# Optimization experiments

Hardware: AMD Instinct MI355X
Metric: run time of the kernel (lower is better)

## Reference

```python
import jax, jax.numpy as jnp
import numpy as np
import math

N = 4096          # ld_num == number of tokens (forced by downsampling Linear over token axis)
D = 640           # input_dim
H = 4             # head_num
E = 16            # per-head output_dim (hardcoded in module)
N_OUT = N // 2    # ld_num // dsp_scale


def setup_inputs() -> dict:
    key = jax.random.key(0)
    ks = jax.random.split(key, 9)
    s = 0.02
    return {
        "x":  jax.random.normal(ks[0], (N, D), dtype=jnp.float32),
        "Wq": jax.random.normal(ks[1], (H, E, D), dtype=jnp.float32) * s,
        "bq": jax.random.normal(ks[2], (H, E), dtype=jnp.float32) * s,
        "Wk": jax.random.normal(ks[3], (H, E, D), dtype=jnp.float32) * s,
        "bk": jax.random.normal(ks[4], (H, E), dtype=jnp.float32) * s,
        "Wv": jax.random.normal(ks[5], (H, E, D), dtype=jnp.float32) * s,
        "bv": jax.random.normal(ks[6], (H, E), dtype=jnp.float32) * s,
        "Wd": jax.random.normal(ks[7], (N_OUT, N), dtype=jnp.float32) * s,
        "bd": jax.random.normal(ks[8], (N_OUT,), dtype=jnp.float32) * s,
    }


def reference(x, Wq, bq, Wk, bk, Wv, bv, Wd, bd):
    # Batched per-head QKV projections: [H, N, E]
    q = jnp.einsum('nd,hed->hne', x, Wq) + bq[:, None, :]
    k = jnp.einsum('nd,hed->hne', x, Wk) + bk[:, None, :]
    v = jnp.einsum('nd,hed->hne', x, Wv) + bv[:, None, :]
    scale = 1.0 / math.sqrt(E)
    attn = jax.nn.softmax(jnp.einsum('hne,hme->hnm', q, k) * scale, axis=-1)  # [H,N,N]
    v = v + jnp.einsum('hnm,hme->hne', attn, v)  # residual + attention readout
    # Concat heads along feature dim: [N, H*E]
    V = jnp.transpose(v, (1, 0, 2)).reshape(N, H * E)
    # downsampling Linear over the token axis, then transpose back: [N//2, H*E]
    out = Wd @ V + bd[:, None]
    return out
```

## Files before the change

### kernel.cpp

```cpp
#include <hip/hip_runtime.h>

typedef __bf16 bf16x8 __attribute__((ext_vector_type(8)));
typedef __bf16 bf16x4 __attribute__((ext_vector_type(4)));
typedef short s16x4 __attribute__((ext_vector_type(4)));
typedef float f32x4 __attribute__((ext_vector_type(4)));

#define MFMA32(a, b, c) __builtin_amdgcn_mfma_f32_16x16x32_bf16((a), (b), (c), 0, 0, 0)
#define MFMA16(a, b, c) __builtin_amdgcn_mfma_f32_16x16x16bf16_1k((a), (b), (c), 0, 0, 0)

#define QSCALE 0.36067376022224085f

static __device__ inline bf16x8 cvt8(float4 a, float4 b) {
    bf16x8 r;
    r[0] = (__bf16)a.x; r[1] = (__bf16)a.y; r[2] = (__bf16)a.z; r[3] = (__bf16)a.w;
    r[4] = (__bf16)b.x; r[5] = (__bf16)b.y; r[6] = (__bf16)b.z; r[7] = (__bf16)b.w;
    return r;
}

__global__ __launch_bounds__(256) void qkv_kernel(
    const float* __restrict__ x,
    const float* __restrict__ Wq, const float* __restrict__ bq,
    const float* __restrict__ Wk, const float* __restrict__ bk,
    const float* __restrict__ Wv, const float* __restrict__ bv,
    const float* __restrict__ bd,
    __bf16* __restrict__ q_bf, __bf16* __restrict__ k_bf,
    __bf16* __restrict__ vT_t, float* __restrict__ out)
{
    __shared__ float red[4 * 4 * 64 * 4];

    const int rg = blockIdx.x & 255;
    const int which = blockIdx.x >> 8;
    const int w  = threadIdx.x >> 6;
    const int lane = threadIdx.x & 63;
    const int c = lane & 15;
    const int g = lane >> 4;
    const int row0 = rg << 4;

    if (which == 0) {
        const int tid0 = (rg << 8) + threadIdx.x;
        const float b = bd[tid0 >> 5];
        *(float2*)(out + (tid0 << 1)) = make_float2(b, b);
    }

    const float* Wsel = (which == 0) ? Wq : (which == 1) ? Wk : Wv;
    const float* bsel = (which == 0) ? bq : (which == 1) ? bk : bv;

    const float* xrow = x + (row0 + c) * 640 + w * 160;
    const float* wr0 = Wsel + (0 * 16 + c) * 640 + w * 160;
    const float* wr1 = Wsel + (1 * 16 + c) * 640 + w * 160;
    const float* wr2 = Wsel + (2 * 16 + c) * 640 + w * 160;
    const float* wr3 = Wsel + (3 * 16 + c) * 640 + w * 160;

    f32x4 acc0 = {0.f,0.f,0.f,0.f}, acc1 = acc0, acc2 = acc0, acc3 = acc0;
    #pragma unroll 5
    for (int k0 = 0; k0 < 160; k0 += 32) {
        const int kk = k0 + (g << 3);
        bf16x8 af = cvt8(*(const float4*)(xrow + kk), *(const float4*)(xrow + kk + 4));
        bf16x8 b0 = cvt8(*(const float4*)(wr0 + kk), *(const float4*)(wr0 + kk + 4));
        bf16x8 b1 = cvt8(*(const float4*)(wr1 + kk), *(const float4*)(wr1 + kk + 4));
        bf16x8 b2 = cvt8(*(const float4*)(wr2 + kk), *(const float4*)(wr2 + kk + 4));
        bf16x8 b3 = cvt8(*(const float4*)(wr3 + kk), *(const float4*)(wr3 + kk + 4));
        acc0 = MFMA32(af, b0, acc0);
        acc1 = MFMA32(af, b1, acc1);
        acc2 = MFMA32(af, b2, acc2);
        acc3 = MFMA32(af, b3, acc3);
    }

    *(f32x4*)&red[((((w << 2) + 0) << 6) + lane) << 2] = acc0;
    *(f32x4*)&red[((((w << 2) + 1) << 6) + lane) << 2] = acc1;
    *(f32x4*)&red[((((w << 2) + 2) << 6) + lane) << 2] = acc2;
    *(f32x4*)&red[((((w << 2) + 3) << 6) + lane) << 2] = acc3;
    __syncthreads();

    const int h = threadIdx.x >> 6;
    f32x4 sum = {0.f,0.f,0.f,0.f};
    #pragma unroll
    for (int ww = 0; ww < 4; ++ww)
        sum += *(const f32x4*)&red[((((ww << 2) + h) << 6) + lane) << 2];

    const float bias = bsel[(h << 4) + c];
    if (which == 2) {
        bf16x4 vv;
        #pragma unroll
        for (int i = 0; i < 4; ++i) vv[i] = (__bf16)(sum[i] + bias);
        *(bf16x4*)(vT_t + ((((h << 8) + rg) << 8) + (c << 4) + (g << 2))) = vv;
    } else {
        #pragma unroll
        for (int i = 0; i < 4; ++i) {
            const int n = row0 + (g << 2) + i;
            const float val = sum[i] + bias;
            if (which == 0) q_bf[(((h << 12) + n) << 4) + c] = (__bf16)(val * QSCALE);
            else            k_bf[(((h << 12) + n) << 4) + c] = (__bf16)val;
        }
    }
}

__global__ __launch_bounds__(512) void attn_kernel(
    const __bf16* __restrict__ q_bf, const __bf16* __restrict__ k_bf,
    const __bf16* __restrict__ vT_t, __bf16* __restrict__ voutT)
{
    __shared__ float accl[8 * 2 * 256];
    __shared__ float lred[8 * 2 * 16];
    __shared__ float ltot[2 * 16];

    const int bx = blockIdx.x;
    const int qp = bx & 127;
    const int h  = bx >> 7;
    const int tid = threadIdx.x;
    const int w = tid >> 6;
    const int lane = tid & 63;
    const int c = lane & 15;
    const int g = lane >> 4;
    const int qbase = qp << 5;

    const s16x4 qf0 = *(const s16x4*)(q_bf + (((h << 12) + qbase + c) << 4) + (g << 2));
    const s16x4 qf1 = *(const s16x4*)(q_bf + (((h << 12) + qbase + 16 + c) << 4) + (g << 2));

    const __bf16* kb = k_bf + (((h << 12) + (w << 9)) << 4) + (c << 4) + (g << 2);
    const __bf16* vb = vT_t + (((h << 8) + (w << 5)) << 8) + (c << 4) + (g << 2);

    bf16x4 one4;
    #pragma unroll
    for (int j = 0; j < 4; ++j) one4[j] = (__bf16)1.0f;
    const s16x4 onesf = __builtin_bit_cast(s16x4, one4);

    const f32x4 z = {0.f, 0.f, 0.f, 0.f};
    f32x4 acc0 = z, acc1 = z, la0 = z, la1 = z;

    s16x4 kr0 = *(const s16x4*)(kb);
    s16x4 kr1 = *(const s16x4*)(kb + 256);
    s16x4 kr2 = *(const s16x4*)(kb + 512);
    s16x4 kr3 = *(const s16x4*)(kb + 768);
    s16x4 vr0 = *(const s16x4*)(vb);
    s16x4 vr1 = *(const s16x4*)(vb + 256);
    s16x4 vr2 = *(const s16x4*)(vb + 512);
    s16x4 vr3 = *(const s16x4*)(vb + 768);

#define ATTN_BODY(KC, VC)                                                     \
    {                                                                         \
        f32x4 s0 = MFMA16((KC), qf0, z);                                      \
        f32x4 s1 = MFMA16((KC), qf1, z);                                      \
        float p00 = __builtin_amdgcn_exp2f(s0[0]);                            \
        float p01 = __builtin_amdgcn_exp2f(s0[1]);                            \
        float p02 = __builtin_amdgcn_exp2f(s0[2]);                            \
        float p03 = __builtin_amdgcn_exp2f(s0[3]);                            \
        float p10 = __builtin_amdgcn_exp2f(s1[0]);                            \
        float p11 = __builtin_amdgcn_exp2f(s1[1]);                            \
        float p12 = __builtin_amdgcn_exp2f(s1[2]);                            \
        float p13 = __builtin_amdgcn_exp2f(s1[3]);                            \
        bf16x4 pb0, pb1;                                                      \
        pb0[0] = (__bf16)p00; pb0[1] = (__bf16)p01;                           \
        pb0[2] = (__bf16)p02; pb0[3] = (__bf16)p03;                           \
        pb1[0] = (__bf16)p10; pb1[1] = (__bf16)p11;                           \
        pb1[2] = (__bf16)p12; pb1[3] = (__bf16)p13;                           \
        const s16x4 pf0 = __builtin_bit_cast(s16x4, pb0);                     \
        const s16x4 pf1 = __builtin_bit_cast(s16x4, pb1);                     \
        la0 = MFMA16(onesf, pf0, la0);                                        \
        la1 = MFMA16(onesf, pf1, la1);                                        \
        acc0 = MFMA16((VC), pf0, acc0);                                       \
        acc1 = MFMA16((VC), pf1, acc1);                                       \
    }

    for (int tt = 0; tt < 32; tt += 4) {
        s16x4 kc, vc;
        kc = kr0; vc = vr0;
        if (tt + 4 < 32) { kr0 = *(const s16x4*)(kb + ((tt + 4) << 8)); vr0 = *(const s16x4*)(vb + ((tt + 4) << 8)); }
        ATTN_BODY(kc, vc)
        kc = kr1; vc = vr1;
        if (tt + 5 < 32) { kr1 = *(const s16x4*)(kb + ((tt + 5) << 8)); vr1 = *(const s16x4*)(vb + ((tt + 5) << 8)); }
        ATTN_BODY(kc, vc)
        kc = kr2; vc = vr2;
        if (tt + 6 < 32) { kr2 = *(const s16x4*)(kb + ((tt + 6) << 8)); vr2 = *(const s16x4*)(vb + ((tt + 6) << 8)); }
        ATTN_BODY(kc, vc)
        kc = kr3; vc = vr3;
        if (tt + 7 < 32) { kr3 = *(const s16x4*)(kb + ((tt + 7) << 8)); vr3 = *(const s16x4*)(vb + ((tt + 7) << 8)); }
        ATTN_BODY(kc, vc)
    }
#undef ATTN_BODY

    *(f32x4*)&accl[(((w << 1) + 0) << 8) + (lane << 2)] = acc0;
    *(f32x4*)&accl[(((w << 1) + 1) << 8) + (lane << 2)] = acc1;
    if (g == 0) {
        lred[(((w << 1) + 0) << 4) + c] = la0[0];
        lred[(((w << 1) + 1) << 4) + c] = la1[0];
    }
    __syncthreads();

    if (tid < 32) {
        const int tile = tid >> 4, cc = tid & 15;
        float s = 0.f;
        #pragma unroll
        for (int w2 = 0; w2 < 8; ++w2) s += lred[(((w2 << 1) + tile) << 4) + cc];
        ltot[(tile << 4) + cc] = 1.0f / s;
    }
    __syncthreads();

    {
        const int tile = tid >> 8;
        const int elem = tid & 255;
        const int lane2 = elem >> 2, i = elem & 3;
        const int c2 = lane2 & 15, g2 = lane2 >> 4;
        const int e = (g2 << 2) + i;
        float s = 0.f;
        #pragma unroll
        for (int w2 = 0; w2 < 8; ++w2) s += accl[(((w2 << 1) + tile) << 8) + elem];
        const int qt = (qp << 1) + tile;
        const float res = (float)vT_t[((((h << 8) + qt) << 8)) + (e << 4) + c2];
        const float val = s * ltot[(tile << 4) + c2] + res;
        voutT[(qp << 11) + (((h << 4) + e) << 5) + (tile << 4) + c2] = (__bf16)val;
    }
}

__global__ __launch_bounds__(256) void dsgemm_kernel(
    const float* __restrict__ Wd, const __bf16* __restrict__ voutT,
    float* __restrict__ out)
{
    const int rb = blockIdx.x & 31;
    const int ks = blockIdx.x >> 5;
    const int w  = threadIdx.x >> 6;
    const int lane = threadIdx.x & 63;
    const int c = lane & 15;
    const int g = lane >> 4;
    const int rowbase = rb * 64 + w * 16;
    const float* wdrow = Wd + (rowbase + c) * 4096;

    f32x4 acc0 = {0.f,0.f,0.f,0.f}, acc1 = acc0, acc2 = acc0, acc3 = acc0;
    #pragma unroll
    for (int it = 0; it < 8; ++it) {
        const int k0 = ks * 256 + it * 32;
        bf16x8 af = cvt8(*(const float4*)(wdrow + k0 + (g << 3)),
                         *(const float4*)(wdrow + k0 + (g << 3) + 4));
        const __bf16* bt = voutT + ((k0 >> 5) << 11) + (g << 3);
        bf16x8 b0 = *(const bf16x8*)(bt + ((c     ) << 5));
        bf16x8 b1 = *(const bf16x8*)(bt + ((c + 16) << 5));
        bf16x8 b2 = *(const bf16x8*)(bt + ((c + 32) << 5));
        bf16x8 b3 = *(const bf16x8*)(bt + ((c + 48) << 5));
        acc0 = MFMA32(af, b0, acc0);
        acc1 = MFMA32(af, b1, acc1);
        acc2 = MFMA32(af, b2, acc2);
        acc3 = MFMA32(af, b3, acc3);
    }

    float* ob = out + rowbase * 64;
    #pragma unroll
    for (int i = 0; i < 4; ++i) {
        const int r = (g << 2) + i;
        atomicAdd(ob + r * 64 +      c, acc0[i]);
        atomicAdd(ob + r * 64 + 16 + c, acc1[i]);
        atomicAdd(ob + r * 64 + 32 + c, acc2[i]);
        atomicAdd(ob + r * 64 + 48 + c, acc3[i]);
    }
}

extern "C" void kernel_launch(void* const* d_in, const int* in_sizes, int n_in,
                              void* d_out, int out_size, void* d_ws, size_t ws_size,
                              hipStream_t stream)
{
    const float* x  = (const float*)d_in[0];
    const float* Wq = (const float*)d_in[1];
    const float* bq = (const float*)d_in[2];
    const float* Wk = (const float*)d_in[3];
    const float* bk = (const float*)d_in[4];
    const float* Wv = (const float*)d_in[5];
    const float* bv = (const float*)d_in[6];
    const float* Wd = (const float*)d_in[7];
    const float* bd = (const float*)d_in[8];
    float* out = (float*)d_out;

    char* ws = (char*)d_ws;
    __bf16* q_bf   = (__bf16*)(ws);
    __bf16* k_bf   = (__bf16*)(ws + (1u << 19));
    __bf16* vT_t   = (__bf16*)(ws + (2u << 19));
    __bf16* voutT  = (__bf16*)(ws + (3u << 19));

    qkv_kernel<<<dim3(768), dim3(256), 0, stream>>>(x, Wq, bq, Wk, bk, Wv, bv, bd,
                                                    q_bf, k_bf, vT_t, out);
    attn_kernel<<<dim3(512), dim3(512), 0, stream>>>(q_bf, k_bf, vT_t, voutT);
    dsgemm_kernel<<<dim3(512), dim3(256), 0, stream>>>(Wd, voutT, out);
}
```

Baseline: 51.51 us.

## Fuse QKV, attention and downsample GEMM into one persistent kernel with grid barriers

Replaces the three launches with a single 256-block persistent kernel. Software grid barriers on atomic counters separate the phases. The QKV phase stages x rows in LDS and computes all three projections per block. Attention blocks now handle 64 queries each instead of 32, and the downsample GEMM writes per-k-split partials that a final phase reduces with the bias, replacing atomicAdd. The aim is to cut launch gaps and atomic contention, at the cost of barrier spin time, an extra memset, lower block parallelism and reliance on all 256 blocks being co-resident.

```diff
diff --git a/kernel.cpp b/kernel.cpp
--- a/kernel.cpp
+++ b/kernel.cpp
@@ -17,238 +17,289 @@
     return r;
 }
 
-__global__ __launch_bounds__(256) void qkv_kernel(
+static __device__ inline void grid_barrier(unsigned* cnt, int nblk) {
+    __syncthreads();
+    if (threadIdx.x == 0) {
+        __threadfence();
+        unsigned prev = __hip_atomic_fetch_add(cnt, 1u, __ATOMIC_ACQ_REL,
+                                               __HIP_MEMORY_SCOPE_AGENT);
+        if ((int)prev + 1 < nblk) {
+            int guard = 0;
+            while (__hip_atomic_load(cnt, __ATOMIC_ACQUIRE,
+                                     __HIP_MEMORY_SCOPE_AGENT) < (unsigned)nblk) {
+                __builtin_amdgcn_s_sleep(8);
+                if (++guard > (1 << 22)) break;
+            }
+        }
+        __threadfence();
+    }
+    __syncthreads();
+}
+
+__global__ __launch_bounds__(512) void fused_kernel(
     const float* __restrict__ x,
     const float* __restrict__ Wq, const float* __restrict__ bq,
     const float* __restrict__ Wk, const float* __restrict__ bk,
     const float* __restrict__ Wv, const float* __restrict__ bv,
-    const float* __restrict__ bd,
+    const float* __restrict__ Wd, const float* __restrict__ bd,
     __bf16* __restrict__ q_bf, __bf16* __restrict__ k_bf,
-    __bf16* __restrict__ vT_t, float* __restrict__ out)
+    __bf16* __restrict__ vT_t, __bf16* __restrict__ voutT,
+    float* __restrict__ partial, unsigned* __restrict__ bars,
+    float* __restrict__ out)
 {
-    __shared__ float red[4 * 4 * 64 * 4];
-
-    const int rg = blockIdx.x & 255;
-    const int which = blockIdx.x >> 8;
-    const int w  = threadIdx.x >> 6;
-    const int lane = threadIdx.x & 63;
-    const int c = lane & 15;
-    const int g = lane >> 4;
-    const int row0 = rg << 4;
-
-    if (which == 0) {
-        const int tid0 = (rg << 8) + threadIdx.x;
-        const float b = bd[tid0 >> 5];
-        *(float2*)(out + (tid0 << 1)) = make_float2(b, b);
-    }
-
-    const float* Wsel = (which == 0) ? Wq : (which == 1) ? Wk : Wv;
-    const float* bsel = (which == 0) ? bq : (which == 1) ? bk : bv;
-
-    const float* xrow = x + (row0 + c) * 640 + w * 160;
-    const float* wr0 = Wsel + (0 * 16 + c) * 640 + w * 160;
-    const float* wr1 = Wsel + (1 * 16 + c) * 640 + w * 160;
-    const float* wr2 = Wsel + (2 * 16 + c) * 640 + w * 160;
-    const float* wr3 = Wsel + (3 * 16 + c) * 640 + w * 160;
-
-    f32x4 acc0 = {0.f,0.f,0.f,0.f}, acc1 = acc0, acc2 = acc0, acc3 = acc0;
-    #pragma unroll 5
-    for (int k0 = 0; k0 < 160; k0 += 32) {
-        const int kk = k0 + (g << 3);
-        bf16x8 af = cvt8(*(const float4*)(xrow + kk), *(const float4*)(xrow + kk + 4));
-        bf16x8 b0 = cvt8(*(const float4*)(wr0 + kk), *(const float4*)(wr0 + kk + 4));
-        bf16x8 b1 = cvt8(*(const float4*)(wr1 + kk), *(const float4*)(wr1 + kk + 4));
-        bf16x8 b2 = cvt8(*(const float4*)(wr2 + kk), *(const float4*)(wr2 + kk + 4));
-        bf16x8 b3 = cvt8(*(const float4*)(wr3 + kk), *(const float4*)(wr3 + kk + 4));
-        acc0 = MFMA32(af, b0, acc0);
-        acc1 = MFMA32(af, b1, acc1);
-        acc2 = MFMA32(af, b2, acc2);
-        acc3 = MFMA32(af, b3, acc3);
-    }
-
-    *(f32x4*)&red[((((w << 2) + 0) << 6) + lane) << 2] = acc0;
-    *(f32x4*)&red[((((w << 2) + 1) << 6) + lane) << 2] = acc1;
-    *(f32x4*)&red[((((w << 2) + 2) << 6) + lane) << 2] = acc2;
-    *(f32x4*)&red[((((w << 2) + 3) << 6) + lane) << 2] = acc3;
-    __syncthreads();
-
-    const int h = threadIdx.x >> 6;
-    f32x4 sum = {0.f,0.f,0.f,0.f};
-    #pragma unroll
-    for (int ww = 0; ww < 4; ++ww)
-        sum += *(const f32x4*)&red[((((ww << 2) + h) << 6) + lane) << 2];
-
-    const float bias = bsel[(h << 4) + c];
-    if (which == 2) {
-        bf16x4 vv;
-        #pragma unroll
-        for (int i = 0; i < 4; ++i) vv[i] = (__bf16)(sum[i] + bias);
-        *(bf16x4*)(vT_t + ((((h << 8) + rg) << 8) + (c << 4) + (g << 2))) = vv;
-    } else {
-        #pragma unroll
-        for (int i = 0; i < 4; ++i) {
-            const int n = row0 + (g << 2) + i;
-            const float val = sum[i] + bias;
-            if (which == 0) q_bf[(((h << 12) + n) << 4) + c] = (__bf16)(val * QSCALE);
-            else            k_bf[(((h << 12) + n) << 4) + c] = (__bf16)val;
-        }
-    }
-}
-
-__global__ __launch_bounds__(512) void attn_kernel(
-    const __bf16* __restrict__ q_bf, const __bf16* __restrict__ k_bf,
-    const __bf16* __restrict__ vT_t, __bf16* __restrict__ voutT)
-{
-    __shared__ float accl[8 * 2 * 256];
-    __shared__ float lred[8 * 2 * 16];
-    __shared__ float ltot[2 * 16];
-
-    const int bx = blockIdx.x;
-    const int qp = bx & 127;
-    const int h  = bx >> 7;
+    __shared__ __align__(16) char arena[67584];
+
     const int tid = threadIdx.x;
     const int w = tid >> 6;
     const int lane = tid & 63;
     const int c = lane & 15;
     const int g = lane >> 4;
-    const int qbase = qp << 5;
-
-    const s16x4 qf0 = *(const s16x4*)(q_bf + (((h << 12) + qbase + c) << 4) + (g << 2));
-    const s16x4 qf1 = *(const s16x4*)(q_bf + (((h << 12) + qbase + 16 + c) << 4) + (g << 2));
-
-    const __bf16* kb = k_bf + (((h << 12) + (w << 9)) << 4) + (c << 4) + (g << 2);
-    const __bf16* vb = vT_t + (((h << 8) + (w << 5)) << 8) + (c << 4) + (g << 2);
-
-    bf16x4 one4;
-    #pragma unroll
-    for (int j = 0; j < 4; ++j) one4[j] = (__bf16)1.0f;
-    const s16x4 onesf = __builtin_bit_cast(s16x4, one4);
-
-    const f32x4 z = {0.f, 0.f, 0.f, 0.f};
-    f32x4 acc0 = z, acc1 = z, la0 = z, la1 = z;
-
-    s16x4 kr0 = *(const s16x4*)(kb);
-    s16x4 kr1 = *(const s16x4*)(kb + 256);
-    s16x4 kr2 = *(const s16x4*)(kb + 512);
-    s16x4 kr3 = *(const s16x4*)(kb + 768);
-    s16x4 vr0 = *(const s16x4*)(vb);
-    s16x4 vr1 = *(const s16x4*)(vb + 256);
-    s16x4 vr2 = *(const s16x4*)(vb + 512);
-    s16x4 vr3 = *(const s16x4*)(vb + 768);
-
+
+    {
+        const int rg = blockIdx.x;
+        const int row0 = rg << 4;
+        float* xs = (float*)arena;
+        f32x4* red = (f32x4*)(arena + 41216);
+
+        const float4* xg = (const float4*)(x + row0 * 640);
+        #pragma unroll
+        for (int i = 0; i < 5; ++i) {
+            const int j = tid + (i << 9);
+            const int row = j / 160, col = j - row * 160;
+            *(float4*)&xs[row * 644 + (col << 2)] = xg[j];
+        }
+        __syncthreads();
+
+        if (w < 6) {
+            const int which = w >> 1, kh = w & 1;
+            const float* Wsel = which == 0 ? Wq : which == 1 ? Wk : Wv;
+            const float* wr0 = Wsel + (0 * 16 + c) * 640 + kh * 320;
+            const float* wr1 = Wsel + (1 * 16 + c) * 640 + kh * 320;
+            const float* wr2 = Wsel + (2 * 16 + c) * 640 + kh * 320;
+            const float* wr3 = Wsel + (3 * 16 + c) * 640 + kh * 320;
+            const float* xr = xs + c * 644 + kh * 320;
+
+            f32x4 acc0 = {0.f,0.f,0.f,0.f}, acc1 = acc0, acc2 = acc0, acc3 = acc0;
+            #pragma unroll 2
+            for (int it = 0; it < 10; ++it) {
+                const int kk = (it << 5) + (g << 3);
+                bf16x8 af = cvt8(*(const float4*)(xr + kk), *(const float4*)(xr + kk + 4));
+                bf16x8 b0 = cvt8(*(const float4*)(wr0 + kk), *(const float4*)(wr0 + kk + 4));
+                bf16x8 b1 = cvt8(*(const float4*)(wr1 + kk), *(const float4*)(wr1 + kk + 4));
+                bf16x8 b2 = cvt8(*(const float4*)(wr2 + kk), *(const float4*)(wr2 + kk + 4));
+                bf16x8 b3 = cvt8(*(const float4*)(wr3 + kk), *(const float4*)(wr3 + kk + 4));
+                acc0 = MFMA32(af, b0, acc0);
+                acc1 = MFMA32(af, b1, acc1);
+                acc2 = MFMA32(af, b2, acc2);
+                acc3 = MFMA32(af, b3, acc3);
+            }
+            red[((w << 2) + 0) * 64 + lane] = acc0;
+            red[((w << 2) + 1) * 64 + lane] = acc1;
+            red[((w << 2) + 2) * 64 + lane] = acc2;
+            red[((w << 2) + 3) * 64 + lane] = acc3;
+        }
+        __syncthreads();
+
+        #pragma unroll
+        for (int pass = 0; pass < 2; ++pass) {
+            const int s = tid + (pass << 9);
+            if (s < 768) {
+                const int which = s >> 8;
+                const int h = (s >> 6) & 3;
+                const int ln = s & 63;
+                const int cc = ln & 15, gg = ln >> 4;
+                f32x4 sum = red[(((which << 1) << 2) + h) * 64 + ln]
+                          + red[((((which << 1) + 1) << 2) + h) * 64 + ln];
+                const float* bsel = which == 0 ? bq : which == 1 ? bk : bv;
+                const float bias = bsel[(h << 4) + cc];
+                if (which == 2) {
+                    bf16x4 vv;
+                    #pragma unroll
+                    for (int i = 0; i < 4; ++i) vv[i] = (__bf16)(sum[i] + bias);
+                    *(bf16x4*)(vT_t + ((((h << 8) + rg) << 8) + (cc << 4) + (gg << 2))) = vv;
+                } else {
+                    #pragma unroll
+                    for (int i = 0; i < 4; ++i) {
+                        const int n = row0 + (gg << 2) + i;
+                        const float val = sum[i] + bias;
+                        if (which == 0) q_bf[(((h << 12) + n) << 4) + cc] = (__bf16)(val * QSCALE);
+                        else            k_bf[(((h << 12) + n) << 4) + cc] = (__bf16)val;
+                    }
+                }
+            }
+        }
+    }
+    grid_barrier(bars + 0, 256);
+
+    {
+        const int h = blockIdx.x >> 6;
+        const int qblk = blockIdx.x & 63;
+        float* accl = (float*)arena;
+        float* lred = (float*)(arena + 32768);
+        float* ltot = (float*)(arena + 34816);
+
+        const int qt0 = qblk << 2;
+        const __bf16* qb = q_bf + (h << 16) + (((qblk << 6) + c) << 4) + (g << 2);
+        const s16x4 qf0 = *(const s16x4*)(qb);
+        const s16x4 qf1 = *(const s16x4*)(qb + 256);
+        const s16x4 qf2 = *(const s16x4*)(qb + 512);
+        const s16x4 qf3 = *(const s16x4*)(qb + 768);
+
+        const __bf16* kb = k_bf + (h << 16) + (w << 13) + (c << 4) + (g << 2);
+        const __bf16* vb = vT_t + (h << 16) + (w << 13) + (c << 4) + (g << 2);
+
+        bf16x4 one4;
+        #pragma unroll
+        for (int j = 0; j < 4; ++j) one4[j] = (__bf16)1.0f;
+        const s16x4 onesf = __builtin_bit_cast(s16x4, one4);
+
+        const f32x4 z = {0.f, 0.f, 0.f, 0.f};
+        f32x4 acc0 = z, acc1 = z, acc2 = z, acc3 = z;
+        f32x4 la0 = z, la1 = z, la2 = z, la3 = z;
+
+        s16x4 kr0 = *(const s16x4*)(kb);
+        s16x4 kr1 = *(const s16x4*)(kb + 256);
+        s16x4 kr2 = *(const s16x4*)(kb + 512);
+        s16x4 kr3 = *(const s16x4*)(kb + 768);
+        s16x4 vr0 = *(const s16x4*)(vb);
+        s16x4 vr1 = *(const s16x4*)(vb + 256);
+        s16x4 vr2 = *(const s16x4*)(vb + 512);
+        s16x4 vr3 = *(const s16x4*)(vb + 768);
+
+#define TILE_OP(QF, ACC, LA, KC, VC)                                          \
+        {                                                                     \
+            f32x4 s_ = MFMA16((KC), (QF), z);                                 \
+            float p0 = __builtin_amdgcn_exp2f(s_[0]);                         \
+            float p1 = __builtin_amdgcn_exp2f(s_[1]);                         \
+            float p2 = __builtin_amdgcn_exp2f(s_[2]);                         \
+            float p3 = __builtin_amdgcn_exp2f(s_[3]);                         \
+            bf16x4 pb;                                                        \
+            pb[0] = (__bf16)p0; pb[1] = (__bf16)p1;                           \
+            pb[2] = (__bf16)p2; pb[3] = (__bf16)p3;                           \
+            const s16x4 pf = __builtin_bit_cast(s16x4, pb);                   \
+            (LA)  = MFMA16(onesf, pf, (LA));                                  \
+            (ACC) = MFMA16((VC), pf, (ACC));                                  \
+        }
 #define ATTN_BODY(KC, VC)                                                     \
-    {                                                                         \
-        f32x4 s0 = MFMA16((KC), qf0, z);                                      \
-        f32x4 s1 = MFMA16((KC), qf1, z);                                      \
-        float p00 = __builtin_amdgcn_exp2f(s0[0]);                            \
-        float p01 = __builtin_amdgcn_exp2f(s0[1]);                            \
-        float p02 = __builtin_amdgcn_exp2f(s0[2]);                            \
-        float p03 = __builtin_amdgcn_exp2f(s0[3]);                            \
-        float p10 = __builtin_amdgcn_exp2f(s1[0]);                            \
-        float p11 = __builtin_amdgcn_exp2f(s1[1]);                            \
-        float p12 = __builtin_amdgcn_exp2f(s1[2]);                            \
-        float p13 = __builtin_amdgcn_exp2f(s1[3]);                            \
-        bf16x4 pb0, pb1;                                                      \
-        pb0[0] = (__bf16)p00; pb0[1] = (__bf16)p01;                           \
-        pb0[2] = (__bf16)p02; pb0[3] = (__bf16)p03;                           \
-        pb1[0] = (__bf16)p10; pb1[1] = (__bf16)p11;                           \
-        pb1[2] = (__bf16)p12; pb1[3] = (__bf16)p13;                           \
-        const s16x4 pf0 = __builtin_bit_cast(s16x4, pb0);                     \
-        const s16x4 pf1 = __builtin_bit_cast(s16x4, pb1);                     \
-        la0 = MFMA16(onesf, pf0, la0);                                        \
-        la1 = MFMA16(onesf, pf1, la1);                                        \
-        acc0 = MFMA16((VC), pf0, acc0);                                       \
-        acc1 = MFMA16((VC), pf1, acc1);                                       \
-    }
-
-    for (int tt = 0; tt < 32; tt += 4) {
-        s16x4 kc, vc;
-        kc = kr0; vc = vr0;
-        if (tt + 4 < 32) { kr0 = *(const s16x4*)(kb + ((tt + 4) << 8)); vr0 = *(const s16x4*)(vb + ((tt + 4) << 8)); }
-        ATTN_BODY(kc, vc)
-        kc = kr1; vc = vr1;
-        if (tt + 5 < 32) { kr1 = *(const s16x4*)(kb + ((tt + 5) << 8)); vr1 = *(const s16x4*)(vb + ((tt + 5) << 8)); }
-        ATTN_BODY(kc, vc)
-        kc = kr2; vc = vr2;
-        if (tt + 6 < 32) { kr2 = *(const s16x4*)(kb + ((tt + 6) << 8)); vr2 = *(const s16x4*)(vb + ((tt + 6) << 8)); }
-        ATTN_BODY(kc, vc)
-        kc = kr3; vc = vr3;
-        if (tt + 7 < 32) { kr3 = *(const s16x4*)(kb + ((tt + 7) << 8)); vr3 = *(const s16x4*)(vb + ((tt + 7) << 8)); }
-        ATTN_BODY(kc, vc)
-    }
+        TILE_OP(qf0, acc0, la0, KC, VC)                                       \
+        TILE_OP(qf1, acc1, la1, KC, VC)                                       \
+        TILE_OP(qf2, acc2, la2, KC, VC)                                       \
+        TILE_OP(qf3, acc3, la3, KC, VC)
+
+        for (int tt = 0; tt < 32; tt += 4) {
+            s16x4 kc, vc;
+            kc = kr0; vc = vr0;
+            if (tt + 4 < 32) { kr0 = *(const s16x4*)(kb + ((tt + 4) << 8)); vr0 = *(const s16x4*)(vb + ((tt + 4) << 8)); }
+            ATTN_BODY(kc, vc)
+            kc = kr1; vc = vr1;
+            if (tt + 5 < 32) { kr1 = *(const s16x4*)(kb + ((tt + 5) << 8)); vr1 = *(const s16x4*)(vb + ((tt + 5) << 8)); }
+            ATTN_BODY(kc, vc)
+            kc = kr2; vc = vr2;
+            if (tt + 6 < 32) { kr2 = *(const s16x4*)(kb + ((tt + 6) << 8)); vr2 = *(const s16x4*)(vb + ((tt + 6) << 8)); }
+            ATTN_BODY(kc, vc)
+            kc = kr3; vc = vr3;
+            if (tt + 7 < 32) { kr3 = *(const s16x4*)(kb + ((tt + 7) << 8)); vr3 = *(const s16x4*)(vb + ((tt + 7) << 8)); }
+            ATTN_BODY(kc, vc)
+        }
 #undef ATTN_BODY
-
-    *(f32x4*)&accl[(((w << 1) + 0) << 8) + (lane << 2)] = acc0;
-    *(f32x4*)&accl[(((w << 1) + 1) << 8) + (lane << 2)] = acc1;
-    if (g == 0) {
-        lred[(((w << 1) + 0) << 4) + c] = la0[0];
-        lred[(((w << 1) + 1) << 4) + c] = la1[0];
-    }
-    __syncthreads();
-
-    if (tid < 32) {
-        const int tile = tid >> 4, cc = tid & 15;
-        float s = 0.f;
-        #pragma unroll
-        for (int w2 = 0; w2 < 8; ++w2) s += lred[(((w2 << 1) + tile) << 4) + cc];
-        ltot[(tile << 4) + cc] = 1.0f / s;
-    }
-    __syncthreads();
+#undef TILE_OP
+
+        *(f32x4*)&accl[(((w << 2) + 0) << 8) + (lane << 2)] = acc0;
+        *(f32x4*)&accl[(((w << 2) + 1) << 8) + (lane << 2)] = acc1;
+        *(f32x4*)&accl[(((w << 2) + 2) << 8) + (lane << 2)] = acc2;
+        *(f32x4*)&accl[(((w << 2) + 3) << 8) + (lane << 2)] = acc3;
+        if (g == 0) {
+            lred[(((w << 2) + 0) << 4) + c] = la0[0];
+            lred[(((w << 2) + 1) << 4) + c] = la1[0];
+            lred[(((w << 2) + 2) << 4) + c] = la2[0];
+            lred[(((w << 2) + 3) << 4) + c] = la3[0];
+        }
+        __syncthreads();
+
+        if (tid < 64) {
+            const int tile = tid >> 4, cc2 = tid & 15;
+            float s = 0.f;
+            #pragma unroll
+            for (int w2 = 0; w2 < 8; ++w2) s += lred[(((w2 << 2) + tile) << 4) + cc2];
+            ltot[tid] = 1.0f / s;
+        }
+        __syncthreads();
+
+        #pragma unroll
+        for (int pass = 0; pass < 2; ++pass) {
+            const int s = tid + (pass << 9);
+            const int tile = s >> 8, elem = s & 255;
+            const int lane2 = elem >> 2, ii = elem & 3;
+            const int c2 = lane2 & 15, g2 = lane2 >> 4;
+            const int e = (g2 << 2) + ii;
+            float ssum = 0.f;
+            #pragma unroll
+            for (int w2 = 0; w2 < 8; ++w2) ssum += accl[(((w2 << 2) + tile) << 8) + elem];
+            const int qt = qt0 + tile;
+            const float res = (float)vT_t[(((h << 8) + qt) << 8) + (e << 4) + c2];
+            const float val = ssum * ltot[(tile << 4) + c2] + res;
+            voutT[((qt >> 1) << 11) + (((h << 4) + e) << 5) + ((qt & 1) << 4) + c2] = (__bf16)val;
+        }
+    }
+    grid_barrier(bars + 16, 256);
 
     {
-        const int tile = tid >> 8;
-        const int elem = tid & 255;
-        const int lane2 = elem >> 2, i = elem & 3;
-        const int c2 = lane2 & 15, g2 = lane2 >> 4;
-        const int e = (g2 << 2) + i;
-        float s = 0.f;
-        #pragma unroll
-        for (int w2 = 0; w2 < 8; ++w2) s += accl[(((w2 << 1) + tile) << 8) + elem];
-        const int qt = (qp << 1) + tile;
-        const float res = (float)vT_t[((((h << 8) + qt) << 8)) + (e << 4) + c2];
-        const float val = s * ltot[(tile << 4) + c2] + res;
-        voutT[(qp << 11) + (((h << 4) + e) << 5) + (tile << 4) + c2] = (__bf16)val;
-    }
-}
-
-__global__ __launch_bounds__(256) void dsgemm_kernel(
-    const float* __restrict__ Wd, const __bf16* __restrict__ voutT,
-    float* __restrict__ out)
-{
-    const int rb = blockIdx.x & 31;
-    const int ks = blockIdx.x >> 5;
-    const int w  = threadIdx.x >> 6;
-    const int lane = threadIdx.x & 63;
-    const int c = lane & 15;
-    const int g = lane >> 4;
-    const int rowbase = rb * 64 + w * 16;
-    const float* wdrow = Wd + (rowbase + c) * 4096;
-
-    f32x4 acc0 = {0.f,0.f,0.f,0.f}, acc1 = acc0, acc2 = acc0, acc3 = acc0;
-    #pragma unroll
-    for (int it = 0; it < 8; ++it) {
-        const int k0 = ks * 256 + it * 32;
-        bf16x8 af = cvt8(*(const float4*)(wdrow + k0 + (g << 3)),
-                         *(const float4*)(wdrow + k0 + (g << 3) + 4));
-        const __bf16* bt = voutT + ((k0 >> 5) << 11) + (g << 3);
-        bf16x8 b0 = *(const bf16x8*)(bt + ((c     ) << 5));
-        bf16x8 b1 = *(const bf16x8*)(bt + ((c + 16) << 5));
-        bf16x8 b2 = *(const bf16x8*)(bt + ((c + 32) << 5));
-        bf16x8 b3 = *(const bf16x8*)(bt + ((c + 48) << 5));
-        acc0 = MFMA32(af, b0, acc0);
-        acc1 = MFMA32(af, b1, acc1);
-        acc2 = MFMA32(af, b2, acc2);
-        acc3 = MFMA32(af, b3, acc3);
-    }
-
-    float* ob = out + rowbase * 64;
-    #pragma unroll
-    for (int i = 0; i < 4; ++i) {
-        const int r = (g << 2) + i;
-        atomicAdd(ob + r * 64 +      c, acc0[i]);
-        atomicAdd(ob + r * 64 + 16 + c, acc1[i]);
-        atomicAdd(ob + r * 64 + 32 + c, acc2[i]);
-        atomicAdd(ob + r * 64 + 48 + c, acc3[i]);
+        const int rb = blockIdx.x >> 3;
+        const int ks = blockIdx.x & 7;
+        const int rsub = w >> 1, kh = w & 1;
+        const int r0 = (rb << 6) + (rsub << 4);
+        const int kb0 = (ks << 9) + (kh << 8);
+        const float* wdrow = Wd + (r0 + c) * 4096 + kb0;
+
+        f32x4 acc0 = {0.f,0.f,0.f,0.f}, acc1 = acc0, acc2 = acc0, acc3 = acc0;
+        #pragma unroll
+        for (int it = 0; it < 8; ++it) {
+            const int k0 = it << 5;
+            bf16x8 af = cvt8(*(const float4*)(wdrow + k0 + (g << 3)),
+                             *(const float4*)(wdrow + k0 + (g << 3) + 4));
+            const __bf16* bt = voutT + (((kb0 + k0) >> 5) << 11) + (g << 3);
+            bf16x8 b0 = *(const bf16x8*)(bt + ((c     ) << 5));
+            bf16x8 b1 = *(const bf16x8*)(bt + ((c + 16) << 5));
+            bf16x8 b2 = *(const bf16x8*)(bt + ((c + 32) << 5));
+            bf16x8 b3 = *(const bf16x8*)(bt + ((c + 48) << 5));
+            acc0 = MFMA32(af, b0, acc0);
+            acc1 = MFMA32(af, b1, acc1);
+            acc2 = MFMA32(af, b2, acc2);
+            acc3 = MFMA32(af, b3, acc3);
+        }
+
+        float* dsred = (float*)arena;
+        if (kh == 1) {
+            *(f32x4*)&dsred[(((rsub << 2) + 0) << 8) + (lane << 2)] = acc0;
+            *(f32x4*)&dsred[(((rsub << 2) + 1) << 8) + (lane << 2)] = acc1;
+            *(f32x4*)&dsred[(((rsub << 2) + 2) << 8) + (lane << 2)] = acc2;
+            *(f32x4*)&dsred[(((rsub << 2) + 3) << 8) + (lane << 2)] = acc3;
+        }
+        __syncthreads();
+        if (kh == 0) {
+            acc0 += *(const f32x4*)&dsred[(((rsub << 2) + 0) << 8) + (lane << 2)];
+            acc1 += *(const f32x4*)&dsred[(((rsub << 2) + 1) << 8) + (lane << 2)];
+            acc2 += *(const f32x4*)&dsred[(((rsub << 2) + 2) << 8) + (lane << 2)];
+            acc3 += *(const f32x4*)&dsred[(((rsub << 2) + 3) << 8) + (lane << 2)];
+            float* pbase = partial + (((ks << 11) + r0) << 6);
+            #pragma unroll
+            for (int i = 0; i < 4; ++i) {
+                const int r = (g << 2) + i;
+                pbase[(r << 6) +      c] = acc0[i];
+                pbase[(r << 6) + 16 + c] = acc1[i];
+                pbase[(r << 6) + 32 + c] = acc2[i];
+                pbase[(r << 6) + 48 + c] = acc3[i];
+            }
+        }
+    }
+    grid_barrier(bars + 32, 256);
+
+    {
+        const int idx = (blockIdx.x << 9) + tid;
+        float s = bd[idx >> 6];
+        #pragma unroll
+        for (int k = 0; k < 8; ++k) s += partial[(k << 17) + idx];
+        out[idx] = s;
     }
 }
 
@@ -272,9 +323,11 @@
     __bf16* k_bf   = (__bf16*)(ws + (1u << 19));
     __bf16* vT_t   = (__bf16*)(ws + (2u << 19));
     __bf16* voutT  = (__bf16*)(ws + (3u << 19));
-
-    qkv_kernel<<<dim3(768), dim3(256), 0, stream>>>(x, Wq, bq, Wk, bk, Wv, bv, bd,
-                                                    q_bf, k_bf, vT_t, out);
-    attn_kernel<<<dim3(512), dim3(512), 0, stream>>>(q_bf, k_bf, vT_t, voutT);
-    dsgemm_kernel<<<dim3(512), dim3(256), 0, stream>>>(Wd, voutT, out);
+    float*  partial = (float*)(ws + (4u << 19));
+    unsigned* bars  = (unsigned*)(ws + (12u << 19));
+
+    hipMemsetAsync(bars, 0, 256, stream);
+    fused_kernel<<<dim3(256), dim3(512), 0, stream>>>(
+        x, Wq, bq, Wk, bk, Wv, bv, Wd, bd,
+        q_bf, k_bf, vT_t, voutT, partial, bars, out);
 }
```

New measurement: 123.4 us. 140% more time.

## Prefetch Wd into cache during attention and replace atomics with partial-sum reduction

Applied to the files above, without the earlier changes.

The attention launch gets 128 extra blocks that read all of Wd (32 MB) and discard the sum, so it sits in the large last-level cache before the downsampling GEMM runs. The GEMM's float atomicAdds into the output are replaced by plain stores of per-K-slice partials, and a new reduce kernel sums the 16 slices and adds the bias, which used to be written in the QKV kernel. This removes atomic contention and hides the Wd fetch behind attention. The cost is an extra launch, an 8 MB partial buffer written and read back, and warm-up blocks that compete with attention for bandwidth and CUs.

```diff
diff --git a/kernel.cpp b/kernel.cpp
--- a/kernel.cpp
+++ b/kernel.cpp
@@ -22,9 +22,8 @@
     const float* __restrict__ Wq, const float* __restrict__ bq,
     const float* __restrict__ Wk, const float* __restrict__ bk,
     const float* __restrict__ Wv, const float* __restrict__ bv,
-    const float* __restrict__ bd,
     __bf16* __restrict__ q_bf, __bf16* __restrict__ k_bf,
-    __bf16* __restrict__ vT_t, float* __restrict__ out)
+    __bf16* __restrict__ vT_t)
 {
     __shared__ float red[4 * 4 * 64 * 4];
 
@@ -35,12 +34,6 @@
     const int c = lane & 15;
     const int g = lane >> 4;
     const int row0 = rg << 4;
-
-    if (which == 0) {
-        const int tid0 = (rg << 8) + threadIdx.x;
-        const float b = bd[tid0 >> 5];
-        *(float2*)(out + (tid0 << 1)) = make_float2(b, b);
-    }
 
     const float* Wsel = (which == 0) ? Wq : (which == 1) ? Wk : Wv;
     const float* bsel = (which == 0) ? bq : (which == 1) ? bk : bv;
@@ -97,16 +90,32 @@
 
 __global__ __launch_bounds__(512) void attn_kernel(
     const __bf16* __restrict__ q_bf, const __bf16* __restrict__ k_bf,
-    const __bf16* __restrict__ vT_t, __bf16* __restrict__ voutT)
+    const __bf16* __restrict__ vT_t, __bf16* __restrict__ voutT,
+    const float* __restrict__ Wd, float* __restrict__ warm_sink)
 {
     __shared__ float accl[8 * 2 * 256];
     __shared__ float lred[8 * 2 * 16];
     __shared__ float ltot[2 * 16];
 
     const int bx = blockIdx.x;
+    const int tid = threadIdx.x;
+
+    if (bx >= 512) {
+        const int wb = bx - 512;
+        const float4* src = (const float4*)Wd;
+        float4 a = {0.f, 0.f, 0.f, 0.f};
+        #pragma unroll 8
+        for (int i = 0; i < 32; ++i) {
+            float4 v = src[(i << 16) + (wb << 9) + tid];
+            a.x += v.x; a.y += v.y; a.z += v.z; a.w += v.w;
+        }
+        const float s = (a.x + a.y) + (a.z + a.w);
+        if (s == 1234.56789f) warm_sink[(wb << 9) + tid] = s;
+        return;
+    }
+
     const int qp = bx & 127;
     const int h  = bx >> 7;
-    const int tid = threadIdx.x;
     const int w = tid >> 6;
     const int lane = tid & 63;
     const int c = lane & 15;
@@ -213,7 +222,7 @@
 
 __global__ __launch_bounds__(256) void dsgemm_kernel(
     const float* __restrict__ Wd, const __bf16* __restrict__ voutT,
-    float* __restrict__ out)
+    float* __restrict__ partial)
 {
     const int rb = blockIdx.x & 31;
     const int ks = blockIdx.x >> 5;
@@ -241,15 +250,28 @@
         acc3 = MFMA32(af, b3, acc3);
     }
 
-    float* ob = out + rowbase * 64;
+    float* pbase = partial + (((ks << 11) + rowbase) << 6);
     #pragma unroll
     for (int i = 0; i < 4; ++i) {
         const int r = (g << 2) + i;
-        atomicAdd(ob + r * 64 +      c, acc0[i]);
-        atomicAdd(ob + r * 64 + 16 + c, acc1[i]);
-        atomicAdd(ob + r * 64 + 32 + c, acc2[i]);
-        atomicAdd(ob + r * 64 + 48 + c, acc3[i]);
-    }
+        pbase[(r << 6) +      c] = acc0[i];
+        pbase[(r << 6) + 16 + c] = acc1[i];
+        pbase[(r << 6) + 32 + c] = acc2[i];
+        pbase[(r << 6) + 48 + c] = acc3[i];
+    }
+}
+
+__global__ __launch_bounds__(256) void reduce_kernel(
+    const float* __restrict__ partial, const float* __restrict__ bd,
+    float* __restrict__ out)
+{
+    const int i4 = blockIdx.x * 256 + threadIdx.x;
+    const float b = bd[i4 >> 4];
+    f32x4 s = {b, b, b, b};
+    #pragma unroll
+    for (int k = 0; k < 16; ++k)
+        s += *(const f32x4*)(partial + (k << 17) + (i4 << 2));
+    *(f32x4*)(out + (i4 << 2)) = s;
 }
 
 extern "C" void kernel_launch(void* const* d_in, const int* in_sizes, int n_in,
@@ -272,9 +294,12 @@
     __bf16* k_bf   = (__bf16*)(ws + (1u << 19));
     __bf16* vT_t   = (__bf16*)(ws + (2u << 19));
     __bf16* voutT  = (__bf16*)(ws + (3u << 19));
-
-    qkv_kernel<<<dim3(768), dim3(256), 0, stream>>>(x, Wq, bq, Wk, bk, Wv, bv, bd,
-                                                    q_bf, k_bf, vT_t, out);
-    attn_kernel<<<dim3(512), dim3(512), 0, stream>>>(q_bf, k_bf, vT_t, voutT);
-    dsgemm_kernel<<<dim3(512), dim3(256), 0, stream>>>(Wd, voutT, out);
-}
+    float*  partial = (float*)(ws + (4u << 19));
+
+    qkv_kernel<<<dim3(768), dim3(256), 0, stream>>>(x, Wq, bq, Wk, bk, Wv, bv,
+                                                    q_bf, k_bf, vT_t);
+    attn_kernel<<<dim3(640), dim3(512), 0, stream>>>(q_bf, k_bf, vT_t, voutT,
+                                                     Wd, partial);
+    dsgemm_kernel<<<dim3(512), dim3(256), 0, stream>>>(Wd, voutT, partial);
+    reduce_kernel<<<dim3(128), dim3(256), 0, stream>>>(partial, bd, out);
+}
```

Result: no change. 51.11 us (-0.8%).
